# Optimization experiments

Hardware: AMD Instinct MI355X
Metric: run time of the kernel (lower is better)

## Reference

```python
import jax, jax.numpy as jnp
import numpy as np

B, L, H, T, S, D = 64, 512, 768, 256, 128, 8
N = B * S            # 8192 graph nodes total
E = 16 * N           # random edges (avg degree 16)
NPD = N // D         # nodes per document
NEG_SLOPE = 0.2


def setup_inputs() -> dict:
    rng = np.random.default_rng(0)
    key = jax.random.key(0)
    ks = jax.random.split(key, 11)
    features = jax.random.normal(ks[0], (B, L, H), jnp.float32)
    starts = rng.integers(0, L - 8, (B, T))
    lens = rng.integers(1, 9, (B, T))
    token_spans = jnp.asarray(np.stack([starts, starts + lens], -1), jnp.int32)
    masks = jnp.ones((B, L), jnp.int32)
    selected_indices = jnp.asarray(rng.integers(0, T, (B, S)), jnp.int32)
    # edges within each document's node block, plus self loops (dgl.add_self_loop)
    dst0 = rng.integers(0, N, E)
    src0 = (dst0 // NPD) * NPD + rng.integers(0, NPD, E)
    loop = np.arange(N)
    src = jnp.asarray(np.concatenate([src0, loop]), jnp.int32)
    dst = jnp.asarray(np.concatenate([dst0, loop]), jnp.int32)
    spd = B // D
    doc_spans = jnp.asarray(
        np.stack([np.arange(D) * spd, (np.arange(D) + 1) * spd], -1), jnp.int32)
    segment_ids = jnp.asarray(rng.integers(0, 2, (B, L)), jnp.int32)
    is_head = jnp.asarray(rng.integers(0, 3, (B, L)), jnp.int32)
    p = lambda k, shp: jax.random.normal(k, shp, jnp.float32) * 0.05
    out = dict(features=features, token_spans=token_spans, masks=masks,
               selected_indices=selected_indices, src=src, dst=dst,
               doc_spans=doc_spans, segment_ids=segment_ids, is_head=is_head)
    for i in range(3):
        out[f"W{i}"] = p(ks[1 + 3 * i], (H, H))
        out[f"al{i}"] = p(ks[2 + 3 * i], (H,))
        out[f"ar{i}"] = p(ks[3 + 3 * i], (H,))
    return out


def _gat_layer(h, W, al, ar, src, dst, n):
    # DGL GATConv, 1 head: z = Wh; e_ij = LeakyReLU(a_l.z_i + a_r.z_j);
    # edge-softmax over incoming edges of each dst; aggregate; ELU.
    z = h @ W                                   # [N, H]
    el = z @ al                                 # [N]
    er = z @ ar                                 # [N]
    e = jax.nn.leaky_relu(el[src] + er[dst], NEG_SLOPE)
    e = e - jax.ops.segment_max(e, dst, num_segments=n)[dst]
    ex = jnp.exp(e)
    a = ex / jax.ops.segment_sum(ex, dst, num_segments=n)[dst]
    out = jax.ops.segment_sum(a[:, None] * z[src], dst, num_segments=n)
    return jax.nn.elu(out)


def reference(features, W0, al0, ar0, W1, al1, ar1, W2, al2, ar2,
              token_spans, masks, selected_indices, src, dst,
              doc_spans, segment_ids, is_head):
    dt = features.dtype
    # --- AverageSpanExtractor over token spans ---
    pos = jnp.arange(L)
    s = token_spans[..., 0:1]                   # [B,T,1]
    e = token_spans[..., 1:2]
    span_mask = ((pos >= s) & (pos < e) & (masks[:, None, :] > 0)).astype(dt)
    counts = jnp.maximum(span_mask.sum(-1), 1.0)
    token_repr = jnp.einsum('btl,blh->bth', span_mask, features) / counts[..., None]
    token_repr = token_repr * (token_spans[..., 1] > 0).astype(dt)[..., None]
    # --- select graph nodes ---
    sel = jnp.take_along_axis(token_repr, selected_indices[:, :, None], axis=1)
    h = sel.reshape(N, H)
    # --- 3-layer single-head GAT ---
    for (W, al, ar) in ((W0, al0, ar0), (W1, al1, ar1), (W2, al2, ar2)):
        h = _gat_layer(h, W, al, ar, src, dst, N)
    # --- dgl.mean_nodes per document ---
    sent_doc = jnp.searchsorted(doc_spans[:, 0], jnp.arange(B), side='right') - 1
    node_doc = sent_doc[jnp.arange(N) // S]
    node_cnt = jnp.maximum(
        jax.ops.segment_sum(jnp.ones(N, dt), node_doc, num_segments=D), 1.0)
    avg = jax.ops.segment_sum(h, node_doc, num_segments=D) / node_cnt[:, None]
    # --- query features ---
    qmask = ((is_head != 2) & (segment_ids == 0) & (masks > 0)).astype(dt)
    all_q = (features * qmask[..., None]).sum(1)   # [B,H]
    doc_cnt = jnp.maximum((doc_spans[:, 1] - doc_spans[:, 0]).astype(dt), 1.0)
    qf = jax.ops.segment_sum(all_q, sent_doc, num_segments=D) / doc_cnt[:, None]
    # --- L1 pairwise distance per document ---
    return jnp.abs(qf - avg).sum(-1)               # [D]
```

## Files before the change

### kernel.cpp

```cpp
#include <hip/hip_runtime.h>
#include <hip/hip_bf16.h>

constexpr int B_ = 64, L_ = 512, H_ = 768, T_ = 256, S_ = 128, D_ = 8;
constexpr int N_ = B_ * S_;
constexpr int E0_ = 16 * N_;
constexpr int NE_ = E0_ + N_;
constexpr float NEG_SLOPE = 0.2f;
constexpr int KDIM = 768;
constexpr int NB_WT = 3 * 576;
constexpr int NB_ZERO = 68;

typedef __attribute__((ext_vector_type(8))) short short8v;
typedef __attribute__((ext_vector_type(4))) float f32x4;

#define GLOAD_LDS16(g, l) __builtin_amdgcn_global_load_lds( \
    (const __attribute__((address_space(1))) void*)(g), \
    (__attribute__((address_space(3))) void*)(l), 16, 0, 0)

__device__ __forceinline__ float bf2f(short s) {
  unsigned u = ((unsigned)(unsigned short)s) << 16;
  return __builtin_bit_cast(float, u);
}
__device__ __forceinline__ short f2bf(float f) {
  return (short)__bfloat16_as_ushort(__float2bfloat16(f));
}
__device__ __forceinline__ int docof(int b, const int* __restrict__ doc_spans) {
  int cnt = 0;
  for (int dd = 0; dd < D_; dd++) cnt += (doc_spans[dd * 2] <= b) ? 1 : 0;
  return cnt - 1;
}

__global__ __launch_bounds__(256) void k_token_wt(const float* __restrict__ features,
                                                  const int* __restrict__ token_spans,
                                                  const int* __restrict__ masks,
                                                  const int* __restrict__ selidx,
                                                  __hip_bfloat16* __restrict__ h0,
                                                  const float* __restrict__ W0,
                                                  const float* __restrict__ W1,
                                                  const float* __restrict__ W2,
                                                  __hip_bfloat16* __restrict__ Wt,
                                                  int4* __restrict__ zero_base) {
  int bid = blockIdx.x;
  if (bid < N_) {
    if (threadIdx.x >= 192) return;
    int n = bid;
    int b = n / S_;
    int t = selidx[n];
    int st = token_spans[(b * T_ + t) * 2 + 0];
    int en = token_spans[(b * T_ + t) * 2 + 1];
    int tid = threadIdx.x;
    float4 a = make_float4(0.f, 0.f, 0.f, 0.f);
    int cnt = 0;
    for (int l = st; l < en; l++) {
      if (masks[b * L_ + l] > 0) {
        cnt++;
        float4 v = ((const float4*)(features + ((size_t)b * L_ + l) * H_))[tid];
        a.x += v.x; a.y += v.y; a.z += v.z; a.w += v.w;
      }
    }
    float sc = (en > 0) ? (1.0f / (float)max(cnt, 1)) : 0.0f;
    short4 o;
    o.x = f2bf(a.x * sc); o.y = f2bf(a.y * sc); o.z = f2bf(a.z * sc); o.w = f2bf(a.w * sc);
    ((short4*)(h0 + (size_t)n * H_))[tid] = o;
    return;
  }
  if (bid < N_ + NB_WT) {
    int wb = bid - N_;
    int layer = wb / 576;
    int rem = wb % 576;
    int k0 = (rem % 24) * 32, n0 = (rem / 24) * 32;
    const float* Ws[3] = {W0, W1, W2};
    const float* W = Ws[layer];
    __hip_bfloat16* O = Wt + (size_t)layer * H_ * H_;
    __shared__ float tbuf[32][33];
    int x = threadIdx.x % 32, y = threadIdx.x / 32;
    for (int i = 0; i < 32; i += 8)
      tbuf[y + i][x] = W[(size_t)(k0 + y + i) * H_ + n0 + x];
    __syncthreads();
    for (int i = 0; i < 32; i += 8)
      O[(size_t)(n0 + y + i) * H_ + k0 + x] = __float2bfloat16(tbuf[x][y + i]);
    return;
  }
  int zi = bid - N_ - NB_WT;
  zero_base[zi * 256 + threadIdx.x] = make_int4(0, 0, 0, 0);
}

__global__ void k_count(const int* __restrict__ dst, int* __restrict__ counts, int ne) {
  int i = blockIdx.x * 256 + threadIdx.x;
  if (i < ne) atomicAdd(&counts[dst[i]], 1);
}

__global__ __launch_bounds__(1024) void k_scan(const int* __restrict__ counts,
                                               int* __restrict__ offs,
                                               int* __restrict__ cursor) {
  __shared__ int part[1024];
  int tid = threadIdx.x;
  int base = tid * 8;
  int loc[8];
  int s = 0;
  for (int i = 0; i < 8; i++) { loc[i] = s; s += counts[base + i]; }
  part[tid] = s;
  __syncthreads();
  for (int off = 1; off < 1024; off <<= 1) {
    int v = (tid >= off) ? part[tid - off] : 0;
    __syncthreads();
    part[tid] += v;
    __syncthreads();
  }
  int excl = (tid == 0) ? 0 : part[tid - 1];
  for (int i = 0; i < 8; i++) {
    int o = excl + loc[i];
    offs[base + i] = o;
    cursor[base + i] = o;
  }
  if (tid == 1023) offs[N_] = part[1023];
}

__global__ void k_scatter(const int* __restrict__ dst, const int* __restrict__ src,
                          int* __restrict__ cursor, int* __restrict__ esrc, int ne) {
  int i = blockIdx.x * 256 + threadIdx.x;
  if (i < ne) { int p = atomicAdd(&cursor[dst[i]], 1); esrc[p] = src[i]; }
}

__global__ __launch_bounds__(256) void k_gemm_bf16(const __hip_bfloat16* __restrict__ A,
                                                   const __hip_bfloat16* __restrict__ Bt,
                                                   unsigned char* __restrict__ C,
                                                   const float* __restrict__ al,
                                                   const float* __restrict__ ar,
                                                   float* __restrict__ el,
                                                   float* __restrict__ er) {
  __shared__ __hip_bfloat16 As[2][128 * 32];
  __shared__ __hip_bfloat16 Bs[2][128 * 32];
  int tid = threadIdx.x;
  int bm = blockIdx.x * 128;
  int bn = blockIdx.y * 128;
  int w = tid >> 6;
  int l = tid & 63;
  int wr = w >> 1, wc = w & 1;
  int lr = l & 15;
  int lk = (l >> 4) * 8;
  f32x4 acc[4][4] = {};

  const __hip_bfloat16* gA[2];
  const __hip_bfloat16* gB[2];
  int ldsoff[2];
#pragma unroll
  for (int i = 0; i < 2; i++) {
    int idx = i * 256 + tid;
    int row = idx >> 2;
    int ck = (idx & 3) * 8;
    gA[i] = A + (size_t)(bm + row) * KDIM + ck;
    gB[i] = Bt + (size_t)(bn + row) * KDIM + ck;
    ldsoff[i] = idx * 8;
  }

  auto stage = [&](int buf, int k0) {
#pragma unroll
    for (int i = 0; i < 2; i++) GLOAD_LDS16(gA[i] + k0, &As[buf][ldsoff[i]]);
#pragma unroll
    for (int i = 0; i < 2; i++) GLOAD_LDS16(gB[i] + k0, &Bs[buf][ldsoff[i]]);
  };

  stage(0, 0);
  __syncthreads();

  constexpr int NT = KDIM / 32;
  for (int t = 0; t < NT; t++) {
    int cur = t & 1;
    if (t < NT - 1) stage(cur ^ 1, (t + 1) * 32);
    short8v a_frag[4], b_frag[4];
#pragma unroll
    for (int m = 0; m < 4; m++)
      a_frag[m] = *(const short8v*)&As[cur][(wr * 64 + m * 16 + lr) * 32 + lk];
#pragma unroll
    for (int n = 0; n < 4; n++)
      b_frag[n] = *(const short8v*)&Bs[cur][(wc * 64 + n * 16 + lr) * 32 + lk];
#pragma unroll
    for (int m = 0; m < 4; m++)
#pragma unroll
      for (int n = 0; n < 4; n++)
        acc[m][n] = __builtin_amdgcn_mfma_f32_16x16x32_bf16(a_frag[m], b_frag[n], acc[m][n], 0, 0, 0);
    __syncthreads();
  }

  float alv[4], arv[4];
#pragma unroll
  for (int n = 0; n < 4; n++) {
    int col = bn + wc * 64 + n * 16 + lr;
    alv[n] = al[col]; arv[n] = ar[col];
  }
#pragma unroll
  for (int m = 0; m < 4; m++) {
    int rbase = bm + wr * 64 + m * 16 + (l >> 4) * 4;
#pragma unroll
    for (int n = 0; n < 4; n++) {
      int col = bn + wc * 64 + n * 16 + lr;
#pragma unroll
      for (int r = 0; r < 4; r++) {
        float v = acc[m][n][r];
        int pk = __builtin_amdgcn_cvt_pk_fp8_f32(v, v, 0, false);
        C[(size_t)(rbase + r) * H_ + col] = (unsigned char)(pk & 0xff);
      }
    }
#pragma unroll
    for (int r = 0; r < 4; r++) {
      float pel = 0.f, per_ = 0.f;
#pragma unroll
      for (int n = 0; n < 4; n++) {
        pel  += acc[m][n][r] * alv[n];
        per_ += acc[m][n][r] * arv[n];
      }
#pragma unroll
      for (int off2 = 1; off2 < 16; off2 <<= 1) {
        pel  += __shfl_xor(pel,  off2);
        per_ += __shfl_xor(per_, off2);
      }
      if (lr == 0) {
        atomicAdd(&el[rbase + r], pel);
        atomicAdd(&er[rbase + r], per_);
      }
    }
  }
}

__global__ __launch_bounds__(256) void k_agg(const unsigned char* __restrict__ z,
                                             const float* __restrict__ el,
                                             const float* __restrict__ er,
                                             const int* __restrict__ offs,
                                             const int* __restrict__ esrc,
                                             __hip_bfloat16* __restrict__ hout) {
  int wv = threadIdx.x >> 6, lane = threadIdx.x & 63;
  int n = blockIdx.x * 4 + wv;
  int o0 = offs[n];
  int deg = offs[n + 1] - o0;
  float ern = er[n];
  float acc[12] = {};

  if (deg <= 64) {
    float w_ = 0.f; int s_ = 0;
    if (lane < deg) {
      s_ = esrc[o0 + lane];
      float v = el[s_] + ern;
      w_ = v > 0.f ? v : NEG_SLOPE * v;
    } else {
      w_ = -1e30f;
    }
    float m = w_;
    for (int off = 32; off; off >>= 1) m = fmaxf(m, __shfl_xor(m, off));
    float ex = (lane < deg) ? __expf(w_ - m) : 0.f;
    float sum = ex;
    for (int off = 32; off; off >>= 1) sum += __shfl_xor(sum, off);
    w_ = ex / sum;
    for (int j = 0; j < deg; j++) {
      float wj = __shfl(w_, j);
      int sj = __shfl(s_, j);
      const unsigned* zr = (const unsigned*)(z + (size_t)sj * H_);
#pragma unroll
      for (int i = 0; i < 3; i++) {
        unsigned u = zr[lane + i * 64];
        acc[i * 4 + 0] += wj * __builtin_amdgcn_cvt_f32_fp8(u, 0);
        acc[i * 4 + 1] += wj * __builtin_amdgcn_cvt_f32_fp8(u, 1);
        acc[i * 4 + 2] += wj * __builtin_amdgcn_cvt_f32_fp8(u, 2);
        acc[i * 4 + 3] += wj * __builtin_amdgcn_cvt_f32_fp8(u, 3);
      }
    }
  } else {
    float lmax = -1e30f;
    for (int i = lane; i < deg; i += 64) {
      float v = el[esrc[o0 + i]] + ern;
      v = v > 0.f ? v : NEG_SLOPE * v;
      lmax = fmaxf(lmax, v);
    }
    for (int off = 32; off; off >>= 1) lmax = fmaxf(lmax, __shfl_xor(lmax, off));
    float lsum = 0.f;
    for (int i = lane; i < deg; i += 64) {
      float v = el[esrc[o0 + i]] + ern;
      v = v > 0.f ? v : NEG_SLOPE * v;
      lsum += __expf(v - lmax);
    }
    for (int off = 32; off; off >>= 1) lsum += __shfl_xor(lsum, off);
    float inv = 1.0f / lsum;
    for (int base = 0; base < deg; base += 64) {
      int chunk = min(64, deg - base);
      float w_ = 0.f; int s_ = 0;
      if (lane < chunk) {
        s_ = esrc[o0 + base + lane];
        float v = el[s_] + ern;
        v = v > 0.f ? v : NEG_SLOPE * v;
        w_ = __expf(v - lmax) * inv;
      }
      for (int j = 0; j < chunk; j++) {
        float wj = __shfl(w_, j);
        int sj = __shfl(s_, j);
        const unsigned* zr = (const unsigned*)(z + (size_t)sj * H_);
#pragma unroll
        for (int i = 0; i < 3; i++) {
          unsigned u = zr[lane + i * 64];
          acc[i * 4 + 0] += wj * __builtin_amdgcn_cvt_f32_fp8(u, 0);
          acc[i * 4 + 1] += wj * __builtin_amdgcn_cvt_f32_fp8(u, 1);
          acc[i * 4 + 2] += wj * __builtin_amdgcn_cvt_f32_fp8(u, 2);
          acc[i * 4 + 3] += wj * __builtin_amdgcn_cvt_f32_fp8(u, 3);
        }
      }
    }
  }

  short4* ho = (short4*)(hout + (size_t)n * H_);
#pragma unroll
  for (int i = 0; i < 3; i++) {
    float e0 = acc[i * 4 + 0]; e0 = e0 > 0.f ? e0 : __expf(e0) - 1.f;
    float e1 = acc[i * 4 + 1]; e1 = e1 > 0.f ? e1 : __expf(e1) - 1.f;
    float e2 = acc[i * 4 + 2]; e2 = e2 > 0.f ? e2 : __expf(e2) - 1.f;
    float e3 = acc[i * 4 + 3]; e3 = e3 > 0.f ? e3 : __expf(e3) - 1.f;
    short4 o; o.x = f2bf(e0); o.y = f2bf(e1); o.z = f2bf(e2); o.w = f2bf(e3);
    ho[lane + i * 64] = o;
  }
}

__global__ __launch_bounds__(192) void k_avgqf(const __hip_bfloat16* __restrict__ h,
                                               const float* __restrict__ features,
                                               const int* __restrict__ masks,
                                               const int* __restrict__ segment_ids,
                                               const int* __restrict__ is_head,
                                               const int* __restrict__ doc_spans,
                                               float* __restrict__ avgp,
                                               float* __restrict__ qfp) {
  int b = blockIdx.x;
  int y = blockIdx.y;
  int tid = threadIdx.x;
  int d = docof(b, doc_spans);
  if (y < 8) {
    int s0 = y * 16;
    float4 a = make_float4(0.f, 0.f, 0.f, 0.f);
    for (int i = 0; i < 16; i++) {
      short4 v = ((const short4*)(h + ((size_t)(b * S_ + s0 + i)) * H_))[tid];
      a.x += bf2f(v.x); a.y += bf2f(v.y); a.z += bf2f(v.z); a.w += bf2f(v.w);
    }
    atomicAdd(&avgp[d * H_ + tid * 4 + 0], a.x);
    atomicAdd(&avgp[d * H_ + tid * 4 + 1], a.y);
    atomicAdd(&avgp[d * H_ + tid * 4 + 2], a.z);
    atomicAdd(&avgp[d * H_ + tid * 4 + 3], a.w);
  } else {
    int l0 = (y - 8) * 64;
    __shared__ float qm[64];
    if (tid < 64) {
      int l = l0 + tid;
      qm[tid] = (is_head[b * L_ + l] != 2 && segment_ids[b * L_ + l] == 0 && masks[b * L_ + l] > 0) ? 1.0f : 0.0f;
    }
    __syncthreads();
    float4 a = make_float4(0.f, 0.f, 0.f, 0.f);
    for (int i = 0; i < 64; i++) {
      if (qm[i] != 0.f) {
        float4 v = ((const float4*)(features + ((size_t)b * L_ + l0 + i) * H_))[tid];
        a.x += v.x; a.y += v.y; a.z += v.z; a.w += v.w;
      }
    }
    atomicAdd(&qfp[d * H_ + tid * 4 + 0], a.x);
    atomicAdd(&qfp[d * H_ + tid * 4 + 1], a.y);
    atomicAdd(&qfp[d * H_ + tid * 4 + 2], a.z);
    atomicAdd(&qfp[d * H_ + tid * 4 + 3], a.w);
  }
}

__global__ __launch_bounds__(512) void k_final(const float* __restrict__ qfp,
                                               const float* __restrict__ avgp,
                                               const int* __restrict__ doc_spans,
                                               float* __restrict__ out) {
  __shared__ int ds[D_ * 2];
  int tid = threadIdx.x;
  if (tid < D_ * 2) ds[tid] = doc_spans[tid];
  __syncthreads();
  int d = tid >> 6, lane = tid & 63;
  int nsent = 0;
  for (int b = 0; b < B_; b++) {
    int cnt = 0;
#pragma unroll
    for (int dd = 0; dd < D_; dd++) cnt += (ds[dd * 2] <= b) ? 1 : 0;
    nsent += ((cnt - 1) == d) ? 1 : 0;
  }
  float inv_node = 1.0f / fmaxf((float)nsent * (float)S_, 1.0f);
  float inv_doc  = 1.0f / fmaxf((float)(ds[d * 2 + 1] - ds[d * 2]), 1.0f);
  float acc = 0.f;
  for (int h = lane; h < H_; h += 64)
    acc += fabsf(qfp[d * H_ + h] * inv_doc - avgp[d * H_ + h] * inv_node);
  for (int off = 32; off; off >>= 1) acc += __shfl_xor(acc, off);
  if (lane == 0) out[d] = acc;
}

extern "C" void kernel_launch(void* const* d_in, const int* in_sizes, int n_in,
                              void* d_out, int out_size, void* d_ws, size_t ws_size,
                              hipStream_t stream) {
  const float* features     = (const float*)d_in[0];
  const int*   token_spans  = (const int*)d_in[1];
  const int*   masks        = (const int*)d_in[2];
  const int*   selidx       = (const int*)d_in[3];
  const int*   src          = (const int*)d_in[4];
  const int*   dst          = (const int*)d_in[5];
  const int*   doc_spans    = (const int*)d_in[6];
  const int*   segment_ids  = (const int*)d_in[7];
  const int*   is_head      = (const int*)d_in[8];
  const float* Wl[3]  = {(const float*)d_in[9],  (const float*)d_in[12], (const float*)d_in[15]};
  const float* alv[3] = {(const float*)d_in[10], (const float*)d_in[13], (const float*)d_in[16]};
  const float* arv[3] = {(const float*)d_in[11], (const float*)d_in[14], (const float*)d_in[17]};
  float* out = (float*)d_out;

  char* ws = (char*)d_ws;
  size_t off = 0;
  auto alloc = [&](size_t bytes) -> void* {
    void* p = ws + off;
    off = (off + bytes + 255) & ~(size_t)255;
    return p;
  };
  __hip_bfloat16* hA = (__hip_bfloat16*)alloc((size_t)N_ * H_ * 2);
  unsigned char*  hB = (unsigned char*)alloc((size_t)N_ * H_);
  __hip_bfloat16* Wt = (__hip_bfloat16*)alloc((size_t)3 * H_ * H_ * 2);
  float* avgp   = (float*)alloc((size_t)2 * D_ * H_ * 4);
  float* qfp    = avgp + (size_t)D_ * H_;
  float* el     = (float*)alloc((size_t)3 * N_ * 4);
  float* er     = (float*)alloc((size_t)3 * N_ * 4);
  int*   counts = (int*)alloc((size_t)N_ * 4);
  int*   offs   = (int*)alloc((size_t)(N_ + 1) * 4);
  int*   cursor = (int*)alloc((size_t)N_ * 4);
  int*   esrc   = (int*)alloc((size_t)NE_ * 4);

  k_token_wt<<<N_ + NB_WT + NB_ZERO, 256, 0, stream>>>(features, token_spans, masks, selidx,
                                                       hA, Wl[0], Wl[1], Wl[2], Wt,
                                                       (int4*)avgp);

  k_count<<<(NE_ + 255) / 256, 256, 0, stream>>>(dst, counts, NE_);
  k_scan<<<1, 1024, 0, stream>>>(counts, offs, cursor);
  k_scatter<<<(NE_ + 255) / 256, 256, 0, stream>>>(dst, src, cursor, esrc, NE_);

  for (int i = 0; i < 3; i++) {
    k_gemm_bf16<<<dim3(N_ / 128, H_ / 128), 256, 0, stream>>>(
        hA, Wt + (size_t)i * H_ * H_, hB, alv[i], arv[i],
        el + (size_t)i * N_, er + (size_t)i * N_);
    k_agg<<<N_ / 4, 256, 0, stream>>>(hB, el + (size_t)i * N_, er + (size_t)i * N_,
                                      offs, esrc, hA);
  }

  k_avgqf<<<dim3(B_, 16), 192, 0, stream>>>(hA, features, masks, segment_ids, is_head,
                                            doc_spans, avgp, qfp);
  k_final<<<1, 512, 0, stream>>>(qfp, avgp, doc_spans, out);
}
```

Measured before the change: 210.3 us.

## Fuse graph build, GAT layers and reductions into one cooperative persistent kernel

Replaces the chain of roughly a dozen kernel launches (count, scan, scatter, three GEMM/aggregate pairs, average/query, final) with a single cooperative kernel of 512 persistent blocks. The stages are separated by grid-wide syncs, and GEMM tiles and aggregation nodes are processed in grid-stride loops. The aim is to remove launch gaps and tail effects between the many small stages. In exchange the scan now runs on one block of 256 threads, the launch needs all blocks co-resident, and each grid.sync adds its own cost. The old multi-kernel path is kept as a fallback if the cooperative launch fails.

```diff
diff --git a/kernel.cpp b/kernel.cpp
--- a/kernel.cpp
+++ b/kernel.cpp
@@ -1,5 +1,8 @@
 #include <hip/hip_runtime.h>
 #include <hip/hip_bf16.h>
+#include <hip/hip_cooperative_groups.h>
+
+namespace cg = cooperative_groups;
 
 constexpr int B_ = 64, L_ = 512, H_ = 768, T_ = 256, S_ = 128, D_ = 8;
 constexpr int N_ = B_ * S_;
@@ -9,6 +12,7 @@
 constexpr int KDIM = 768;
 constexpr int NB_WT = 3 * 576;
 constexpr int NB_ZERO = 68;
+constexpr int MEGA_GRID = 512;
 
 typedef __attribute__((ext_vector_type(8))) short short8v;
 typedef __attribute__((ext_vector_type(4))) float f32x4;
@@ -85,6 +89,335 @@
   zero_base[zi * 256 + threadIdx.x] = make_int4(0, 0, 0, 0);
 }
 
+__device__ __forceinline__ void gemm_tile_body(
+    int bm, int bn, int tid, int wv, int lane,
+    const __hip_bfloat16* __restrict__ hA, const __hip_bfloat16* __restrict__ Bt,
+    unsigned char* __restrict__ hB,
+    const float* __restrict__ al, const float* __restrict__ ar,
+    float* __restrict__ elp, float* __restrict__ erp,
+    short (*smA)[128 * 32], short (*smB)[128 * 32]) {
+  int wr = wv >> 1, wc = wv & 1;
+  int lr = lane & 15;
+  int lk = (lane >> 4) * 8;
+  f32x4 acc[4][4] = {};
+
+  const __hip_bfloat16* gA[2];
+  const __hip_bfloat16* gB[2];
+  int ldsoff[2];
+#pragma unroll
+  for (int i = 0; i < 2; i++) {
+    int idx = i * 256 + tid;
+    int row = idx >> 2;
+    int ck = (idx & 3) * 8;
+    gA[i] = hA + (size_t)(bm + row) * KDIM + ck;
+    gB[i] = Bt + (size_t)(bn + row) * KDIM + ck;
+    ldsoff[i] = idx * 8;
+  }
+#pragma unroll
+  for (int i = 0; i < 2; i++) GLOAD_LDS16(gA[i], &smA[0][ldsoff[i]]);
+#pragma unroll
+  for (int i = 0; i < 2; i++) GLOAD_LDS16(gB[i], &smB[0][ldsoff[i]]);
+  __syncthreads();
+
+  constexpr int NT = KDIM / 32;
+  for (int t = 0; t < NT; t++) {
+    int cur = t & 1;
+    if (t < NT - 1) {
+      int k0 = (t + 1) * 32;
+#pragma unroll
+      for (int i = 0; i < 2; i++) GLOAD_LDS16(gA[i] + k0, &smA[cur ^ 1][ldsoff[i]]);
+#pragma unroll
+      for (int i = 0; i < 2; i++) GLOAD_LDS16(gB[i] + k0, &smB[cur ^ 1][ldsoff[i]]);
+    }
+    short8v a_frag[4], b_frag[4];
+#pragma unroll
+    for (int m = 0; m < 4; m++)
+      a_frag[m] = *(const short8v*)&smA[cur][(wr * 64 + m * 16 + lr) * 32 + lk];
+#pragma unroll
+    for (int n = 0; n < 4; n++)
+      b_frag[n] = *(const short8v*)&smB[cur][(wc * 64 + n * 16 + lr) * 32 + lk];
+#pragma unroll
+    for (int m = 0; m < 4; m++)
+#pragma unroll
+      for (int n = 0; n < 4; n++)
+        acc[m][n] = __builtin_amdgcn_mfma_f32_16x16x32_bf16(a_frag[m], b_frag[n], acc[m][n], 0, 0, 0);
+    __syncthreads();
+  }
+
+  float alv[4], arv[4];
+#pragma unroll
+  for (int n = 0; n < 4; n++) {
+    int col = bn + wc * 64 + n * 16 + lr;
+    alv[n] = al[col]; arv[n] = ar[col];
+  }
+#pragma unroll
+  for (int m = 0; m < 4; m++) {
+    int rbase = bm + wr * 64 + m * 16 + (lane >> 4) * 4;
+#pragma unroll
+    for (int n = 0; n < 4; n++) {
+      int col = bn + wc * 64 + n * 16 + lr;
+#pragma unroll
+      for (int r = 0; r < 4; r++) {
+        float v = acc[m][n][r];
+        int pk = __builtin_amdgcn_cvt_pk_fp8_f32(v, v, 0, false);
+        hB[(size_t)(rbase + r) * H_ + col] = (unsigned char)(pk & 0xff);
+      }
+    }
+#pragma unroll
+    for (int r = 0; r < 4; r++) {
+      float pel = 0.f, per_ = 0.f;
+#pragma unroll
+      for (int n = 0; n < 4; n++) {
+        pel  += acc[m][n][r] * alv[n];
+        per_ += acc[m][n][r] * arv[n];
+      }
+#pragma unroll
+      for (int off2 = 1; off2 < 16; off2 <<= 1) {
+        pel  += __shfl_xor(pel,  off2);
+        per_ += __shfl_xor(per_, off2);
+      }
+      if (lr == 0) {
+        atomicAdd(&elp[rbase + r], pel);
+        atomicAdd(&erp[rbase + r], per_);
+      }
+    }
+  }
+}
+
+__device__ __forceinline__ void agg_node_body(
+    int n, int lane,
+    const unsigned char* __restrict__ hB,
+    const float* __restrict__ elp, const float* __restrict__ erp,
+    const int* __restrict__ offs, const int* __restrict__ esrc,
+    __hip_bfloat16* __restrict__ hA) {
+  int o0 = offs[n];
+  int deg = offs[n + 1] - o0;
+  float ern = erp[n];
+  float acc[12] = {};
+
+  if (deg <= 64) {
+    float w_ = 0.f; int s_ = 0;
+    if (lane < deg) {
+      s_ = esrc[o0 + lane];
+      float v = elp[s_] + ern;
+      w_ = v > 0.f ? v : NEG_SLOPE * v;
+    } else {
+      w_ = -1e30f;
+    }
+    float m = w_;
+    for (int off2 = 32; off2; off2 >>= 1) m = fmaxf(m, __shfl_xor(m, off2));
+    float ex = (lane < deg) ? __expf(w_ - m) : 0.f;
+    float sum = ex;
+    for (int off2 = 32; off2; off2 >>= 1) sum += __shfl_xor(sum, off2);
+    w_ = ex / sum;
+    for (int j = 0; j < deg; j++) {
+      float wj = __shfl(w_, j);
+      int sj = __shfl(s_, j);
+      const unsigned* zr = (const unsigned*)(hB + (size_t)sj * H_);
+#pragma unroll
+      for (int i = 0; i < 3; i++) {
+        unsigned u = zr[lane + i * 64];
+        acc[i * 4 + 0] += wj * __builtin_amdgcn_cvt_f32_fp8(u, 0);
+        acc[i * 4 + 1] += wj * __builtin_amdgcn_cvt_f32_fp8(u, 1);
+        acc[i * 4 + 2] += wj * __builtin_amdgcn_cvt_f32_fp8(u, 2);
+        acc[i * 4 + 3] += wj * __builtin_amdgcn_cvt_f32_fp8(u, 3);
+      }
+    }
+  } else {
+    float lmax = -1e30f;
+    for (int i = lane; i < deg; i += 64) {
+      float v = elp[esrc[o0 + i]] + ern;
+      v = v > 0.f ? v : NEG_SLOPE * v;
+      lmax = fmaxf(lmax, v);
+    }
+    for (int off2 = 32; off2; off2 >>= 1) lmax = fmaxf(lmax, __shfl_xor(lmax, off2));
+    float lsum = 0.f;
+    for (int i = lane; i < deg; i += 64) {
+      float v = elp[esrc[o0 + i]] + ern;
+      v = v > 0.f ? v : NEG_SLOPE * v;
+      lsum += __expf(v - lmax);
+    }
+    for (int off2 = 32; off2; off2 >>= 1) lsum += __shfl_xor(lsum, off2);
+    float inv = 1.0f / lsum;
+    for (int base = 0; base < deg; base += 64) {
+      int chunk = min(64, deg - base);
+      float w_ = 0.f; int s_ = 0;
+      if (lane < chunk) {
+        s_ = esrc[o0 + base + lane];
+        float v = elp[s_] + ern;
+        v = v > 0.f ? v : NEG_SLOPE * v;
+        w_ = __expf(v - lmax) * inv;
+      }
+      for (int j = 0; j < chunk; j++) {
+        float wj = __shfl(w_, j);
+        int sj = __shfl(s_, j);
+        const unsigned* zr = (const unsigned*)(hB + (size_t)sj * H_);
+#pragma unroll
+        for (int i = 0; i < 3; i++) {
+          unsigned u = zr[lane + i * 64];
+          acc[i * 4 + 0] += wj * __builtin_amdgcn_cvt_f32_fp8(u, 0);
+          acc[i * 4 + 1] += wj * __builtin_amdgcn_cvt_f32_fp8(u, 1);
+          acc[i * 4 + 2] += wj * __builtin_amdgcn_cvt_f32_fp8(u, 2);
+          acc[i * 4 + 3] += wj * __builtin_amdgcn_cvt_f32_fp8(u, 3);
+        }
+      }
+    }
+  }
+
+  short4* ho = (short4*)(hA + (size_t)n * H_);
+#pragma unroll
+  for (int i = 0; i < 3; i++) {
+    float e0 = acc[i * 4 + 0]; e0 = e0 > 0.f ? e0 : __expf(e0) - 1.f;
+    float e1 = acc[i * 4 + 1]; e1 = e1 > 0.f ? e1 : __expf(e1) - 1.f;
+    float e2 = acc[i * 4 + 2]; e2 = e2 > 0.f ? e2 : __expf(e2) - 1.f;
+    float e3 = acc[i * 4 + 3]; e3 = e3 > 0.f ? e3 : __expf(e3) - 1.f;
+    short4 o; o.x = f2bf(e0); o.y = f2bf(e1); o.z = f2bf(e2); o.w = f2bf(e3);
+    ho[lane + i * 64] = o;
+  }
+}
+
+__global__ __launch_bounds__(256, 2) void k_mega(
+    const int* __restrict__ dstv, const int* __restrict__ srcv,
+    int* __restrict__ counts, int* __restrict__ offs, int* __restrict__ cursor,
+    int* __restrict__ esrc,
+    __hip_bfloat16* __restrict__ hA, unsigned char* __restrict__ hB,
+    const __hip_bfloat16* __restrict__ Wt,
+    const float* __restrict__ al0, const float* __restrict__ ar0,
+    const float* __restrict__ al1, const float* __restrict__ ar1,
+    const float* __restrict__ al2, const float* __restrict__ ar2,
+    float* __restrict__ el, float* __restrict__ er,
+    const float* __restrict__ features, const int* __restrict__ masks,
+    const int* __restrict__ segment_ids, const int* __restrict__ is_head,
+    const int* __restrict__ doc_spans,
+    float* __restrict__ avgp, float* __restrict__ qfp, float* __restrict__ out) {
+  cg::grid_group grid = cg::this_grid();
+  int tid = threadIdx.x;
+  int wv = tid >> 6, lane = tid & 63;
+
+  __shared__ union SM {
+    struct { short A[2][128 * 32]; short B[2][128 * 32]; } g;
+    int part[256];
+    float qm[64];
+  } sm;
+
+  for (int i = blockIdx.x * 256 + tid; i < NE_; i += MEGA_GRID * 256)
+    atomicAdd(&counts[dstv[i]], 1);
+  grid.sync();
+
+  if (blockIdx.x == 0) {
+    int base = tid * 32;
+    int s = 0;
+    for (int i = 0; i < 32; i++) s += counts[base + i];
+    sm.part[tid] = s;
+    __syncthreads();
+    for (int off2 = 1; off2 < 256; off2 <<= 1) {
+      int v = (tid >= off2) ? sm.part[tid - off2] : 0;
+      __syncthreads();
+      sm.part[tid] += v;
+      __syncthreads();
+    }
+    int run = tid ? sm.part[tid - 1] : 0;
+    for (int i = 0; i < 32; i++) {
+      offs[base + i] = run;
+      cursor[base + i] = run;
+      run += counts[base + i];
+    }
+    if (tid == 255) offs[N_] = run;
+  }
+  grid.sync();
+
+  for (int i = blockIdx.x * 256 + tid; i < NE_; i += MEGA_GRID * 256) {
+    int p = atomicAdd(&cursor[dstv[i]], 1);
+    esrc[p] = srcv[i];
+  }
+  grid.sync();
+
+#pragma unroll 1
+  for (int layer = 0; layer < 3; layer++) {
+    const float* al = layer == 0 ? al0 : (layer == 1 ? al1 : al2);
+    const float* ar = layer == 0 ? ar0 : (layer == 1 ? ar1 : ar2);
+    float* elp = el + layer * N_;
+    float* erp = er + layer * N_;
+    const __hip_bfloat16* Bt = Wt + (size_t)layer * H_ * H_;
+
+    constexpr int NTILE = (N_ / 128) * (H_ / 128);
+    for (int tile = blockIdx.x; tile < NTILE; tile += MEGA_GRID) {
+      int bm = (tile % (N_ / 128)) * 128;
+      int bn = (tile / (N_ / 128)) * 128;
+      gemm_tile_body(bm, bn, tid, wv, lane, hA, Bt, hB, al, ar, elp, erp, sm.g.A, sm.g.B);
+    }
+    grid.sync();
+
+    for (int g = blockIdx.x; g < N_ / 4; g += MEGA_GRID)
+      agg_node_body(g * 4 + wv, lane, hB, elp, erp, offs, esrc, hA);
+    grid.sync();
+  }
+
+  for (int u = blockIdx.x; u < 1024; u += MEGA_GRID) {
+    if (u < 512) {
+      int b = u >> 3, s0 = (u & 7) * 16;
+      if (tid < 192) {
+        float4 a = make_float4(0.f, 0.f, 0.f, 0.f);
+        for (int i = 0; i < 16; i++) {
+          short4 v = ((const short4*)(hA + ((size_t)(b * S_ + s0 + i)) * H_))[tid];
+          a.x += bf2f(v.x); a.y += bf2f(v.y); a.z += bf2f(v.z); a.w += bf2f(v.w);
+        }
+        int d = docof(b, doc_spans);
+        atomicAdd(&avgp[d * H_ + tid * 4 + 0], a.x);
+        atomicAdd(&avgp[d * H_ + tid * 4 + 1], a.y);
+        atomicAdd(&avgp[d * H_ + tid * 4 + 2], a.z);
+        atomicAdd(&avgp[d * H_ + tid * 4 + 3], a.w);
+      }
+    } else {
+      int vq = u - 512;
+      int b = vq >> 3, l0 = (vq & 7) * 64;
+      __syncthreads();
+      if (tid < 64) {
+        int l = l0 + tid;
+        sm.qm[tid] = (is_head[b * L_ + l] != 2 && segment_ids[b * L_ + l] == 0 && masks[b * L_ + l] > 0) ? 1.0f : 0.0f;
+      }
+      __syncthreads();
+      if (tid < 192) {
+        float4 a = make_float4(0.f, 0.f, 0.f, 0.f);
+        for (int i = 0; i < 64; i++) {
+          if (sm.qm[i] != 0.f) {
+            float4 v = ((const float4*)(features + ((size_t)b * L_ + l0 + i) * H_))[tid];
+            a.x += v.x; a.y += v.y; a.z += v.z; a.w += v.w;
+          }
+        }
+        int d = docof(b, doc_spans);
+        atomicAdd(&qfp[d * H_ + tid * 4 + 0], a.x);
+        atomicAdd(&qfp[d * H_ + tid * 4 + 1], a.y);
+        atomicAdd(&qfp[d * H_ + tid * 4 + 2], a.z);
+        atomicAdd(&qfp[d * H_ + tid * 4 + 3], a.w);
+      }
+    }
+  }
+  grid.sync();
+
+  if (blockIdx.x == 0) {
+    int ds[16];
+#pragma unroll
+    for (int i = 0; i < 16; i++) ds[i] = doc_spans[i];
+    for (int d = wv; d < D_; d += 4) {
+      int nsent = 0;
+      for (int b = 0; b < B_; b++) {
+        int cnt = 0;
+#pragma unroll
+        for (int dd = 0; dd < D_; dd++) cnt += (ds[dd * 2] <= b) ? 1 : 0;
+        nsent += ((cnt - 1) == d) ? 1 : 0;
+      }
+      float inv_node = 1.0f / fmaxf((float)nsent * (float)S_, 1.0f);
+      float inv_doc  = 1.0f / fmaxf((float)(ds[d * 2 + 1] - ds[d * 2]), 1.0f);
+      float acc = 0.f;
+      for (int h = lane; h < H_; h += 64)
+        acc += fabsf(qfp[d * H_ + h] * inv_doc - avgp[d * H_ + h] * inv_node);
+      for (int off2 = 32; off2; off2 >>= 1) acc += __shfl_xor(acc, off2);
+      if (lane == 0) out[d] = acc;
+    }
+  }
+}
+
 __global__ void k_count(const int* __restrict__ dst, int* __restrict__ counts, int ne) {
   int i = blockIdx.x * 256 + threadIdx.x;
   if (i < ne) atomicAdd(&counts[dst[i]], 1);
@@ -129,98 +462,11 @@
                                                    const float* __restrict__ ar,
                                                    float* __restrict__ el,
                                                    float* __restrict__ er) {
-  __shared__ __hip_bfloat16 As[2][128 * 32];
-  __shared__ __hip_bfloat16 Bs[2][128 * 32];
+  __shared__ short As[2][128 * 32];
+  __shared__ short Bs[2][128 * 32];
   int tid = threadIdx.x;
-  int bm = blockIdx.x * 128;
-  int bn = blockIdx.y * 128;
-  int w = tid >> 6;
-  int l = tid & 63;
-  int wr = w >> 1, wc = w & 1;
-  int lr = l & 15;
-  int lk = (l >> 4) * 8;
-  f32x4 acc[4][4] = {};
-
-  const __hip_bfloat16* gA[2];
-  const __hip_bfloat16* gB[2];
-  int ldsoff[2];
-#pragma unroll
-  for (int i = 0; i < 2; i++) {
-    int idx = i * 256 + tid;
-    int row = idx >> 2;
-    int ck = (idx & 3) * 8;
-    gA[i] = A + (size_t)(bm + row) * KDIM + ck;
-    gB[i] = Bt + (size_t)(bn + row) * KDIM + ck;
-    ldsoff[i] = idx * 8;
-  }
-
-  auto stage = [&](int buf, int k0) {
-#pragma unroll
-    for (int i = 0; i < 2; i++) GLOAD_LDS16(gA[i] + k0, &As[buf][ldsoff[i]]);
-#pragma unroll
-    for (int i = 0; i < 2; i++) GLOAD_LDS16(gB[i] + k0, &Bs[buf][ldsoff[i]]);
-  };
-
-  stage(0, 0);
-  __syncthreads();
-
-  constexpr int NT = KDIM / 32;
-  for (int t = 0; t < NT; t++) {
-    int cur = t & 1;
-    if (t < NT - 1) stage(cur ^ 1, (t + 1) * 32);
-    short8v a_frag[4], b_frag[4];
-#pragma unroll
-    for (int m = 0; m < 4; m++)
-      a_frag[m] = *(const short8v*)&As[cur][(wr * 64 + m * 16 + lr) * 32 + lk];
-#pragma unroll
-    for (int n = 0; n < 4; n++)
-      b_frag[n] = *(const short8v*)&Bs[cur][(wc * 64 + n * 16 + lr) * 32 + lk];
-#pragma unroll
-    for (int m = 0; m < 4; m++)
-#pragma unroll
-      for (int n = 0; n < 4; n++)
-        acc[m][n] = __builtin_amdgcn_mfma_f32_16x16x32_bf16(a_frag[m], b_frag[n], acc[m][n], 0, 0, 0);
-    __syncthreads();
-  }
-
-  float alv[4], arv[4];
-#pragma unroll
-  for (int n = 0; n < 4; n++) {
-    int col = bn + wc * 64 + n * 16 + lr;
-    alv[n] = al[col]; arv[n] = ar[col];
-  }
-#pragma unroll
-  for (int m = 0; m < 4; m++) {
-    int rbase = bm + wr * 64 + m * 16 + (l >> 4) * 4;
-#pragma unroll
-    for (int n = 0; n < 4; n++) {
-      int col = bn + wc * 64 + n * 16 + lr;
-#pragma unroll
-      for (int r = 0; r < 4; r++) {
-        float v = acc[m][n][r];
-        int pk = __builtin_amdgcn_cvt_pk_fp8_f32(v, v, 0, false);
-        C[(size_t)(rbase + r) * H_ + col] = (unsigned char)(pk & 0xff);
-      }
-    }
-#pragma unroll
-    for (int r = 0; r < 4; r++) {
-      float pel = 0.f, per_ = 0.f;
-#pragma unroll
-      for (int n = 0; n < 4; n++) {
-        pel  += acc[m][n][r] * alv[n];
-        per_ += acc[m][n][r] * arv[n];
-      }
-#pragma unroll
-      for (int off2 = 1; off2 < 16; off2 <<= 1) {
-        pel  += __shfl_xor(pel,  off2);
-        per_ += __shfl_xor(per_, off2);
-      }
-      if (lr == 0) {
-        atomicAdd(&el[rbase + r], pel);
-        atomicAdd(&er[rbase + r], per_);
-      }
-    }
-  }
+  gemm_tile_body(blockIdx.x * 128, blockIdx.y * 128, tid, tid >> 6, tid & 63,
+                 A, Bt, C, al, ar, el, er, As, Bs);
 }
 
 __global__ __launch_bounds__(256) void k_agg(const unsigned char* __restrict__ z,
@@ -230,91 +476,7 @@
                                              const int* __restrict__ esrc,
                                              __hip_bfloat16* __restrict__ hout) {
   int wv = threadIdx.x >> 6, lane = threadIdx.x & 63;
-  int n = blockIdx.x * 4 + wv;
-  int o0 = offs[n];
-  int deg = offs[n + 1] - o0;
-  float ern = er[n];
-  float acc[12] = {};
-
-  if (deg <= 64) {
-    float w_ = 0.f; int s_ = 0;
-    if (lane < deg) {
-      s_ = esrc[o0 + lane];
-      float v = el[s_] + ern;
-      w_ = v > 0.f ? v : NEG_SLOPE * v;
-    } else {
-      w_ = -1e30f;
-    }
-    float m = w_;
-    for (int off = 32; off; off >>= 1) m = fmaxf(m, __shfl_xor(m, off));
-    float ex = (lane < deg) ? __expf(w_ - m) : 0.f;
-    float sum = ex;
-    for (int off = 32; off; off >>= 1) sum += __shfl_xor(sum, off);
-    w_ = ex / sum;
-    for (int j = 0; j < deg; j++) {
-      float wj = __shfl(w_, j);
-      int sj = __shfl(s_, j);
-      const unsigned* zr = (const unsigned*)(z + (size_t)sj * H_);
-#pragma unroll
-      for (int i = 0; i < 3; i++) {
-        unsigned u = zr[lane + i * 64];
-        acc[i * 4 + 0] += wj * __builtin_amdgcn_cvt_f32_fp8(u, 0);
-        acc[i * 4 + 1] += wj * __builtin_amdgcn_cvt_f32_fp8(u, 1);
-        acc[i * 4 + 2] += wj * __builtin_amdgcn_cvt_f32_fp8(u, 2);
-        acc[i * 4 + 3] += wj * __builtin_amdgcn_cvt_f32_fp8(u, 3);
-      }
-    }
-  } else {
-    float lmax = -1e30f;
-    for (int i = lane; i < deg; i += 64) {
-      float v = el[esrc[o0 + i]] + ern;
-      v = v > 0.f ? v : NEG_SLOPE * v;
-      lmax = fmaxf(lmax, v);
-    }
-    for (int off = 32; off; off >>= 1) lmax = fmaxf(lmax, __shfl_xor(lmax, off));
-    float lsum = 0.f;
-    for (int i = lane; i < deg; i += 64) {
-      float v = el[esrc[o0 + i]] + ern;
-      v = v > 0.f ? v : NEG_SLOPE * v;
-      lsum += __expf(v - lmax);
-    }
-    for (int off = 32; off; off >>= 1) lsum += __shfl_xor(lsum, off);
-    float inv = 1.0f / lsum;
-    for (int base = 0; base < deg; base += 64) {
-      int chunk = min(64, deg - base);
-      float w_ = 0.f; int s_ = 0;
-      if (lane < chunk) {
-        s_ = esrc[o0 + base + lane];
-        float v = el[s_] + ern;
-        v = v > 0.f ? v : NEG_SLOPE * v;
-        w_ = __expf(v - lmax) * inv;
-      }
-      for (int j = 0; j < chunk; j++) {
-        float wj = __shfl(w_, j);
-        int sj = __shfl(s_, j);
-        const unsigned* zr = (const unsigned*)(z + (size_t)sj * H_);
-#pragma unroll
-        for (int i = 0; i < 3; i++) {
-          unsigned u = zr[lane + i * 64];
-          acc[i * 4 + 0] += wj * __builtin_amdgcn_cvt_f32_fp8(u, 0);
-          acc[i * 4 + 1] += wj * __builtin_amdgcn_cvt_f32_fp8(u, 1);
-          acc[i * 4 + 2] += wj * __builtin_amdgcn_cvt_f32_fp8(u, 2);
-          acc[i * 4 + 3] += wj * __builtin_amdgcn_cvt_f32_fp8(u, 3);
-        }
-      }
-    }
-  }
-
-  short4* ho = (short4*)(hout + (size_t)n * H_);
-#pragma unroll
-  for (int i = 0; i < 3; i++) {
-    float e0 = acc[i * 4 + 0]; e0 = e0 > 0.f ? e0 : __expf(e0) - 1.f;
-    float e1 = acc[i * 4 + 1]; e1 = e1 > 0.f ? e1 : __expf(e1) - 1.f;
-    float e2 = acc[i * 4 + 2]; e2 = e2 > 0.f ? e2 : __expf(e2) - 1.f;
-    float e3 = acc[i * 4 + 3]; e3 = e3 > 0.f ? e3 : __expf(e3) - 1.f;
-    short4 o; o.x = f2bf(e0); o.y = f2bf(e1); o.z = f2bf(e2); o.w = f2bf(e3);
-    ho[lane + i * 64] = o;
-  }
+  agg_node_body(blockIdx.x * 4 + wv, lane, z, el, er, offs, esrc, hout);
 }
 
 __global__ __launch_bounds__(192) void k_avgqf(const __hip_bfloat16* __restrict__ h,
@@ -399,9 +561,15 @@
   const int*   doc_spans    = (const int*)d_in[6];
   const int*   segment_ids  = (const int*)d_in[7];
   const int*   is_head      = (const int*)d_in[8];
-  const float* Wl[3]  = {(const float*)d_in[9],  (const float*)d_in[12], (const float*)d_in[15]};
-  const float* alv[3] = {(const float*)d_in[10], (const float*)d_in[13], (const float*)d_in[16]};
-  const float* arv[3] = {(const float*)d_in[11], (const float*)d_in[14], (const float*)d_in[17]};
+  const float* W0  = (const float*)d_in[9];
+  const float* al0 = (const float*)d_in[10];
+  const float* ar0 = (const float*)d_in[11];
+  const float* W1  = (const float*)d_in[12];
+  const float* al1 = (const float*)d_in[13];
+  const float* ar1 = (const float*)d_in[14];
+  const float* W2  = (const float*)d_in[15];
+  const float* al2 = (const float*)d_in[16];
+  const float* ar2 = (const float*)d_in[17];
   float* out = (float*)d_out;
 
   char* ws = (char*)d_ws;
@@ -424,22 +592,34 @@
   int*   esrc   = (int*)alloc((size_t)NE_ * 4);
 
   k_token_wt<<<N_ + NB_WT + NB_ZERO, 256, 0, stream>>>(features, token_spans, masks, selidx,
-                                                       hA, Wl[0], Wl[1], Wl[2], Wt,
+                                                       hA, W0, W1, W2, Wt,
                                                        (int4*)avgp);
 
-  k_count<<<(NE_ + 255) / 256, 256, 0, stream>>>(dst, counts, NE_);
-  k_scan<<<1, 1024, 0, stream>>>(counts, offs, cursor);
-  k_scatter<<<(NE_ + 255) / 256, 256, 0, stream>>>(dst, src, cursor, esrc, NE_);
-
-  for (int i = 0; i < 3; i++) {
-    k_gemm_bf16<<<dim3(N_ / 128, H_ / 128), 256, 0, stream>>>(
-        hA, Wt + (size_t)i * H_ * H_, hB, alv[i], arv[i],
-        el + (size_t)i * N_, er + (size_t)i * N_);
-    k_agg<<<N_ / 4, 256, 0, stream>>>(hB, el + (size_t)i * N_, er + (size_t)i * N_,
-                                      offs, esrc, hA);
-  }
-
-  k_avgqf<<<dim3(B_, 16), 192, 0, stream>>>(hA, features, masks, segment_ids, is_head,
-                                            doc_spans, avgp, qfp);
-  k_final<<<1, 512, 0, stream>>>(qfp, avgp, doc_spans, out);
-}
+  void* args[] = {
+    (void*)&dst, (void*)&src, (void*)&counts, (void*)&offs, (void*)&cursor, (void*)&esrc,
+    (void*)&hA, (void*)&hB, (void*)&Wt,
+    (void*)&al0, (void*)&ar0, (void*)&al1, (void*)&ar1, (void*)&al2, (void*)&ar2,
+    (void*)&el, (void*)&er,
+    (void*)&features, (void*)&masks, (void*)&segment_ids, (void*)&is_head, (void*)&doc_spans,
+    (void*)&avgp, (void*)&qfp, (void*)&out
+  };
+  hipError_t cerr = hipLaunchCooperativeKernel((void*)k_mega, dim3(MEGA_GRID), dim3(256),
+                                               args, 0, stream);
+  if (cerr != hipSuccess) {
+    k_count<<<(NE_ + 255) / 256, 256, 0, stream>>>(dst, counts, NE_);
+    k_scan<<<1, 1024, 0, stream>>>(counts, offs, cursor);
+    k_scatter<<<(NE_ + 255) / 256, 256, 0, stream>>>(dst, src, cursor, esrc, NE_);
+    const float* alv[3] = {al0, al1, al2};
+    const float* arv[3] = {ar0, ar1, ar2};
+    for (int i = 0; i < 3; i++) {
+      k_gemm_bf16<<<dim3(N_ / 128, H_ / 128), 256, 0, stream>>>(
+          hA, Wt + (size_t)i * H_ * H_, hB, alv[i], arv[i],
+          el + (size_t)i * N_, er + (size_t)i * N_);
+      k_agg<<<N_ / 4, 256, 0, stream>>>(hB, el + (size_t)i * N_, er + (size_t)i * N_,
+                                        offs, esrc, hA);
+    }
+    k_avgqf<<<dim3(B_, 16), 192, 0, stream>>>(hA, features, masks, segment_ids, is_head,
+                                              doc_spans, avgp, qfp);
+    k_final<<<1, 512, 0, stream>>>(qfp, avgp, doc_spans, out);
+  }
+}
```

Measured after the change: 829.8 us. +294.6%, slower.

## Fuse count/scan and avg/final via last-block tickets, move query sum into prep

Applied to the files above, without the earlier changes.

Merges the edge-count and prefix-scan kernels into one: the last block to finish, found with an atomic ticket counter, performs the scan. It also fuses the node-mean and final L1-distance kernels the same way. The query-feature partial sums move into the early prep kernel, writing per-chunk partials instead of atomics, and the aggregation kernel's block order is swizzled. Together these cut two kernel launches and shorten the tail of the pipeline. In exchange, the tail work runs in a single block serially over partials, and ticket counters must be zeroed on every call.

```diff
diff --git a/kernel.cpp b/kernel.cpp
--- a/kernel.cpp
+++ b/kernel.cpp
@@ -8,7 +8,8 @@
 constexpr float NEG_SLOPE = 0.2f;
 constexpr int KDIM = 768;
 constexpr int NB_WT = 3 * 576;
-constexpr int NB_ZERO = 68;
+constexpr int NB_ZERO = 63;
+constexpr int NB_QF = 512;
 
 typedef __attribute__((ext_vector_type(8))) short short8v;
 typedef __attribute__((ext_vector_type(4))) float f32x4;
@@ -29,17 +30,23 @@
   for (int dd = 0; dd < D_; dd++) cnt += (doc_spans[dd * 2] <= b) ? 1 : 0;
   return cnt - 1;
 }
-
-__global__ __launch_bounds__(256) void k_token_wt(const float* __restrict__ features,
-                                                  const int* __restrict__ token_spans,
-                                                  const int* __restrict__ masks,
-                                                  const int* __restrict__ selidx,
-                                                  __hip_bfloat16* __restrict__ h0,
-                                                  const float* __restrict__ W0,
-                                                  const float* __restrict__ W1,
-                                                  const float* __restrict__ W2,
-                                                  __hip_bfloat16* __restrict__ Wt,
-                                                  int4* __restrict__ zero_base) {
+__device__ __forceinline__ float aload(const float* p) {
+  return __hip_atomic_load(p, __ATOMIC_RELAXED, __HIP_MEMORY_SCOPE_AGENT);
+}
+
+__global__ __launch_bounds__(256) void k_prep(const float* __restrict__ features,
+                                              const int* __restrict__ token_spans,
+                                              const int* __restrict__ masks,
+                                              const int* __restrict__ selidx,
+                                              __hip_bfloat16* __restrict__ h0,
+                                              const float* __restrict__ W0,
+                                              const float* __restrict__ W1,
+                                              const float* __restrict__ W2,
+                                              __hip_bfloat16* __restrict__ Wt,
+                                              int4* __restrict__ zero_base,
+                                              const int* __restrict__ segment_ids,
+                                              const int* __restrict__ is_head,
+                                              float* __restrict__ qpart) {
   int bid = blockIdx.x;
   if (bid < N_) {
     if (threadIdx.x >= 192) return;
@@ -81,39 +88,72 @@
       O[(size_t)(n0 + y + i) * H_ + k0 + x] = __float2bfloat16(tbuf[x][y + i]);
     return;
   }
-  int zi = bid - N_ - NB_WT;
-  zero_base[zi * 256 + threadIdx.x] = make_int4(0, 0, 0, 0);
-}
-
-__global__ void k_count(const int* __restrict__ dst, int* __restrict__ counts, int ne) {
+  if (bid < N_ + NB_WT + NB_ZERO) {
+    int zi = bid - N_ - NB_WT;
+    zero_base[zi * 256 + threadIdx.x] = make_int4(0, 0, 0, 0);
+    return;
+  }
+  {
+    int q = bid - N_ - NB_WT - NB_ZERO;
+    int b = q >> 3, l0 = (q & 7) * 64;
+    int tid = threadIdx.x;
+    if (tid >= 192) return;
+    __shared__ float qm[64];
+    if (tid < 64) {
+      int l = l0 + tid;
+      qm[tid] = (is_head[b * L_ + l] != 2 && segment_ids[b * L_ + l] == 0 && masks[b * L_ + l] > 0) ? 1.0f : 0.0f;
+    }
+    __syncthreads();
+    float4 a = make_float4(0.f, 0.f, 0.f, 0.f);
+    for (int i = 0; i < 64; i++) {
+      if (qm[i] != 0.f) {
+        float4 v = ((const float4*)(features + ((size_t)b * L_ + l0 + i) * H_))[tid];
+        a.x += v.x; a.y += v.y; a.z += v.z; a.w += v.w;
+      }
+    }
+    ((float4*)(qpart + (size_t)q * H_))[tid] = a;
+  }
+}
+
+__global__ __launch_bounds__(256) void k_count_scan(const int* __restrict__ dst,
+                                                    int* __restrict__ counts,
+                                                    int* __restrict__ offs,
+                                                    int* __restrict__ cursor,
+                                                    int* __restrict__ tickets) {
   int i = blockIdx.x * 256 + threadIdx.x;
-  if (i < ne) atomicAdd(&counts[dst[i]], 1);
-}
-
-__global__ __launch_bounds__(1024) void k_scan(const int* __restrict__ counts,
-                                               int* __restrict__ offs,
-                                               int* __restrict__ cursor) {
-  __shared__ int part[1024];
-  int tid = threadIdx.x;
-  int base = tid * 8;
-  int loc[8];
+  if (i < NE_) atomicAdd(&counts[dst[i]], 1);
+  __threadfence();
+  __syncthreads();
+  __shared__ int lastf;
+  if (threadIdx.x == 0)
+    lastf = (atomicAdd(&tickets[0], 1) == (int)gridDim.x - 1) ? 1 : 0;
+  __syncthreads();
+  if (!lastf) return;
+  __shared__ int part[256];
+  int base = threadIdx.x * 32;
+  int c[32];
   int s = 0;
-  for (int i = 0; i < 8; i++) { loc[i] = s; s += counts[base + i]; }
-  part[tid] = s;
-  __syncthreads();
-  for (int off = 1; off < 1024; off <<= 1) {
-    int v = (tid >= off) ? part[tid - off] : 0;
+#pragma unroll
+  for (int j = 0; j < 32; j++) {
+    c[j] = __hip_atomic_load(&counts[base + j], __ATOMIC_RELAXED, __HIP_MEMORY_SCOPE_AGENT);
+    s += c[j];
+  }
+  part[threadIdx.x] = s;
+  __syncthreads();
+  for (int off = 1; off < 256; off <<= 1) {
+    int v = (threadIdx.x >= off) ? part[threadIdx.x - off] : 0;
     __syncthreads();
-    part[tid] += v;
+    part[threadIdx.x] += v;
     __syncthreads();
   }
-  int excl = (tid == 0) ? 0 : part[tid - 1];
-  for (int i = 0; i < 8; i++) {
-    int o = excl + loc[i];
-    offs[base + i] = o;
-    cursor[base + i] = o;
-  }
-  if (tid == 1023) offs[N_] = part[1023];
+  int run = threadIdx.x ? part[threadIdx.x - 1] : 0;
+#pragma unroll
+  for (int j = 0; j < 32; j++) {
+    offs[base + j] = run;
+    cursor[base + j] = run;
+    run += c[j];
+  }
+  if (threadIdx.x == 255) offs[N_] = run;
 }
 
 __global__ void k_scatter(const int* __restrict__ dst, const int* __restrict__ src,
@@ -229,8 +269,9 @@
                                              const int* __restrict__ offs,
                                              const int* __restrict__ esrc,
                                              __hip_bfloat16* __restrict__ hout) {
+  int nb = ((blockIdx.x & 7) << 8) + (blockIdx.x >> 3);
   int wv = threadIdx.x >> 6, lane = threadIdx.x & 63;
-  int n = blockIdx.x * 4 + wv;
+  int n = nb * 4 + wv;
   int o0 = offs[n];
   int deg = offs[n + 1] - o0;
   float ern = er[n];
@@ -317,74 +358,58 @@
   }
 }
 
-__global__ __launch_bounds__(192) void k_avgqf(const __hip_bfloat16* __restrict__ h,
-                                               const float* __restrict__ features,
-                                               const int* __restrict__ masks,
-                                               const int* __restrict__ segment_ids,
-                                               const int* __restrict__ is_head,
-                                               const int* __restrict__ doc_spans,
-                                               float* __restrict__ avgp,
-                                               float* __restrict__ qfp) {
-  int b = blockIdx.x;
-  int y = blockIdx.y;
+__global__ __launch_bounds__(192) void k_avg_final(const __hip_bfloat16* __restrict__ h,
+                                                   const int* __restrict__ doc_spans,
+                                                   float* __restrict__ avgp,
+                                                   const float* __restrict__ qpart,
+                                                   float* __restrict__ out,
+                                                   int* __restrict__ tickets) {
+  int b = blockIdx.x >> 3;
+  int s0 = (blockIdx.x & 7) * 16;
   int tid = threadIdx.x;
-  int d = docof(b, doc_spans);
-  if (y < 8) {
-    int s0 = y * 16;
+  {
     float4 a = make_float4(0.f, 0.f, 0.f, 0.f);
     for (int i = 0; i < 16; i++) {
       short4 v = ((const short4*)(h + ((size_t)(b * S_ + s0 + i)) * H_))[tid];
       a.x += bf2f(v.x); a.y += bf2f(v.y); a.z += bf2f(v.z); a.w += bf2f(v.w);
     }
+    int d = docof(b, doc_spans);
     atomicAdd(&avgp[d * H_ + tid * 4 + 0], a.x);
     atomicAdd(&avgp[d * H_ + tid * 4 + 1], a.y);
     atomicAdd(&avgp[d * H_ + tid * 4 + 2], a.z);
     atomicAdd(&avgp[d * H_ + tid * 4 + 3], a.w);
-  } else {
-    int l0 = (y - 8) * 64;
-    __shared__ float qm[64];
-    if (tid < 64) {
-      int l = l0 + tid;
-      qm[tid] = (is_head[b * L_ + l] != 2 && segment_ids[b * L_ + l] == 0 && masks[b * L_ + l] > 0) ? 1.0f : 0.0f;
-    }
-    __syncthreads();
-    float4 a = make_float4(0.f, 0.f, 0.f, 0.f);
-    for (int i = 0; i < 64; i++) {
-      if (qm[i] != 0.f) {
-        float4 v = ((const float4*)(features + ((size_t)b * L_ + l0 + i) * H_))[tid];
-        a.x += v.x; a.y += v.y; a.z += v.z; a.w += v.w;
-      }
-    }
-    atomicAdd(&qfp[d * H_ + tid * 4 + 0], a.x);
-    atomicAdd(&qfp[d * H_ + tid * 4 + 1], a.y);
-    atomicAdd(&qfp[d * H_ + tid * 4 + 2], a.z);
-    atomicAdd(&qfp[d * H_ + tid * 4 + 3], a.w);
-  }
-}
-
-__global__ __launch_bounds__(512) void k_final(const float* __restrict__ qfp,
-                                               const float* __restrict__ avgp,
-                                               const int* __restrict__ doc_spans,
-                                               float* __restrict__ out) {
-  __shared__ int ds[D_ * 2];
-  int tid = threadIdx.x;
-  if (tid < D_ * 2) ds[tid] = doc_spans[tid];
-  __syncthreads();
-  int d = tid >> 6, lane = tid & 63;
-  int nsent = 0;
-  for (int b = 0; b < B_; b++) {
-    int cnt = 0;
-#pragma unroll
-    for (int dd = 0; dd < D_; dd++) cnt += (ds[dd * 2] <= b) ? 1 : 0;
-    nsent += ((cnt - 1) == d) ? 1 : 0;
-  }
-  float inv_node = 1.0f / fmaxf((float)nsent * (float)S_, 1.0f);
-  float inv_doc  = 1.0f / fmaxf((float)(ds[d * 2 + 1] - ds[d * 2]), 1.0f);
-  float acc = 0.f;
-  for (int h = lane; h < H_; h += 64)
-    acc += fabsf(qfp[d * H_ + h] * inv_doc - avgp[d * H_ + h] * inv_node);
-  for (int off = 32; off; off >>= 1) acc += __shfl_xor(acc, off);
-  if (lane == 0) out[d] = acc;
+  }
+  __threadfence();
+  __syncthreads();
+  __shared__ int lastf;
+  if (tid == 0)
+    lastf = (atomicAdd(&tickets[1], 1) == (int)gridDim.x - 1) ? 1 : 0;
+  __syncthreads();
+  if (!lastf) return;
+
+  int lane = tid & 63;
+  for (int d = tid >> 6; d < D_; d += 3) {
+    int nsent = 0;
+    for (int bb = 0; bb < B_; bb++)
+      nsent += (docof(bb, doc_spans) == d) ? 1 : 0;
+    float inv_node = 1.0f / fmaxf((float)nsent * (float)S_, 1.0f);
+    float inv_doc  = 1.0f / fmaxf((float)(doc_spans[d * 2 + 1] - doc_spans[d * 2]), 1.0f);
+    float acc = 0.f;
+    for (int hh = lane; hh < H_; hh += 64) {
+      float qa = 0.f;
+      for (int bb = 0; bb < B_; bb++) {
+        if (docof(bb, doc_spans) == d) {
+          const float* qp = qpart + (size_t)bb * 8 * H_ + hh;
+#pragma unroll
+          for (int c = 0; c < 8; c++) qa += qp[(size_t)c * H_];
+        }
+      }
+      float av = aload(&avgp[d * H_ + hh]);
+      acc += fabsf(qa * inv_doc - av * inv_node);
+    }
+    for (int off = 32; off; off >>= 1) acc += __shfl_xor(acc, off);
+    if (lane == 0) out[d] = acc;
+  }
 }
 
 extern "C" void kernel_launch(void* const* d_in, const int* in_sizes, int n_in,
@@ -414,21 +439,21 @@
   __hip_bfloat16* hA = (__hip_bfloat16*)alloc((size_t)N_ * H_ * 2);
   unsigned char*  hB = (unsigned char*)alloc((size_t)N_ * H_);
   __hip_bfloat16* Wt = (__hip_bfloat16*)alloc((size_t)3 * H_ * H_ * 2);
-  float* avgp   = (float*)alloc((size_t)2 * D_ * H_ * 4);
-  float* qfp    = avgp + (size_t)D_ * H_;
-  float* el     = (float*)alloc((size_t)3 * N_ * 4);
-  float* er     = (float*)alloc((size_t)3 * N_ * 4);
-  int*   counts = (int*)alloc((size_t)N_ * 4);
+  float* avgp    = (float*)alloc((size_t)D_ * H_ * 4);
+  float* el      = (float*)alloc((size_t)3 * N_ * 4);
+  float* er      = (float*)alloc((size_t)3 * N_ * 4);
+  int*   counts  = (int*)alloc((size_t)N_ * 4);
+  int*   tickets = (int*)alloc((size_t)4096);
+  float* qpart  = (float*)alloc((size_t)NB_QF * H_ * 4);
   int*   offs   = (int*)alloc((size_t)(N_ + 1) * 4);
   int*   cursor = (int*)alloc((size_t)N_ * 4);
   int*   esrc   = (int*)alloc((size_t)NE_ * 4);
 
-  k_token_wt<<<N_ + NB_WT + NB_ZERO, 256, 0, stream>>>(features, token_spans, masks, selidx,
-                                                       hA, Wl[0], Wl[1], Wl[2], Wt,
-                                                       (int4*)avgp);
-
-  k_count<<<(NE_ + 255) / 256, 256, 0, stream>>>(dst, counts, NE_);
-  k_scan<<<1, 1024, 0, stream>>>(counts, offs, cursor);
+  k_prep<<<N_ + NB_WT + NB_ZERO + NB_QF, 256, 0, stream>>>(
+      features, token_spans, masks, selidx, hA, Wl[0], Wl[1], Wl[2], Wt,
+      (int4*)avgp, segment_ids, is_head, qpart);
+
+  k_count_scan<<<(NE_ + 255) / 256, 256, 0, stream>>>(dst, counts, offs, cursor, tickets);
   k_scatter<<<(NE_ + 255) / 256, 256, 0, stream>>>(dst, src, cursor, esrc, NE_);
 
   for (int i = 0; i < 3; i++) {
@@ -439,7 +464,5 @@
                                       offs, esrc, hA);
   }
 
-  k_avgqf<<<dim3(B_, 16), 192, 0, stream>>>(hA, features, masks, segment_ids, is_head,
-                                            doc_spans, avgp, qfp);
-  k_final<<<1, 512, 0, stream>>>(qfp, avgp, doc_spans, out);
-}
+  k_avg_final<<<B_ * 8, 192, 0, stream>>>(hA, doc_spans, avgp, qpart, out, tickets);
+}
```

Result: slower. 558.3 us (+165.5%).
